# Kernel tuning notes

Measured on AMD Instinct MI355X. Metric: run time of the kernel, lower is better.

Reference implementation:

```python
import jax, jax.numpy as jnp
import numpy as np

EPS = 1e-8


def _mp_match(v1, v2, w):
    """Fused multi-perspective cosine match.
    v1, v2: (G, L, D); w: (P, D). Returns (G, L, P).
    cos_p(l) = <w_p*v1_l, w_p*v2_l> / max(||w_p*v1_l|| * ||w_p*v2_l||, eps)
    """
    w2 = w * w  # (P, D)
    num = jnp.einsum('gld,pd->glp', v1 * v2, w2)
    n1 = jnp.sqrt(jnp.einsum('gld,pd->glp', v1 * v1, w2))
    n2 = jnp.sqrt(jnp.einsum('gld,pd->glp', v2 * v2, w2))
    return num / jnp.maximum(n1 * n2, EPS)


def setup_inputs() -> dict:
    key = jax.random.key(0)
    k1, k2 = jax.random.split(key)
    n_graphs = 64
    nodes_per_graph = 2048
    dim = 128  # must equal perspectives (mp_w is square)
    N = n_graphs * nodes_per_graph
    feats = jax.random.normal(k1, (N, dim), dtype=jnp.float32)
    graph_idx = jnp.repeat(jnp.arange(n_graphs, dtype=jnp.int64), nodes_per_graph)
    mp_w = jax.random.uniform(k2, (dim, dim), dtype=jnp.float32)  # torch.rand
    return {"feats": feats, "mp_w": mp_w, "graph_idx": graph_idx, "n_graphs": n_graphs}


def reference(feats, mp_w, graph_idx, n_graphs):
    N, d = feats.shape
    L = N // n_graphs  # equal-size graphs, graph_idx is sorted/contiguous
    g = feats.reshape(n_graphs, L, d)
    p = g[0::2]  # (G/2, L, d) premise graphs
    h = g[1::2]  # (G/2, L, d) hypothesis graphs
    # cosine_attention is a plain dot product (no normalization in source)
    att = jnp.einsum('gld,gmd->glm', p, h)        # (G/2, Lp, Lh)
    att_p = jnp.einsum('glm,gmd->gld', att, h)     # (G/2, Lp, d)
    att_h = jnp.einsum('glm,gld->gmd', att, p)     # (G/2, Lh, d)
    multi_p = _mp_match(p, att_p, mp_w)            # (G/2, Lp, P)
    multi_h = _mp_match(h, att_h, mp_w)            # (G/2, Lh, P)
    # original concatenates [p0, h0, p1, h1, ...] along node axis
    P = mp_w.shape[0]
    out = jnp.stack([multi_p, multi_h], axis=1).reshape(n_graphs * L, P)
    return out
```

## Files before the change

kernel.cpp:

```cpp
#include <hip/hip_runtime.h>
#include <math.h>

#define D 128
#define GRAPHS 64

typedef __attribute__((ext_vector_type(8))) short bf16x8;
typedef __attribute__((ext_vector_type(4))) float f32x4;

union U4H8 { uint4 u; bf16x8 h; };

__device__ __forceinline__ unsigned short f2bf(float f) {
  union { float f; unsigned u; } v; v.f = f;
  unsigned r = v.u + 0x7fffu + ((v.u >> 16) & 1u);
  return (unsigned short)(r >> 16);
}
__device__ __forceinline__ unsigned asu(float f) {
  union { float f; unsigned u; } v; v.f = f; return v.u;
}
__device__ __forceinline__ float asf(unsigned u) {
  union { unsigned u; float f; } v; v.u = u; return v.f;
}

__global__ __launch_bounds__(256, 2) void gram_partial_kernel(
    const float* __restrict__ feats, unsigned short* __restrict__ partial,
    int L, int KS) {
  const int g = blockIdx.x / KS;
  const int sl = blockIdx.x - g * KS;
  const int chunk = L / KS;
  const float* __restrict__ X = feats + ((size_t)g * L + (size_t)sl * chunk) * D;

  __shared__ __align__(16) unsigned short smem[16384];
  const int tid = threadIdx.x;
  const int wv = tid >> 6, lane = tid & 63, quad = lane >> 4, ln = lane & 15;

  f32x4 acc[2][8];
#pragma unroll
  for (int rt = 0; rt < 2; ++rt)
#pragma unroll
    for (int ct = 0; ct < 8; ++ct) acc[rt][ct] = (f32x4)(0.f);

  int k2v[4], d4v[4];
#pragma unroll
  for (int v = 0; v < 4; ++v) {
    int tt = tid + v * 256;
    k2v[v] = tt & 31;
    d4v[v] = tt >> 5;
  }
  float4 pf[8];
#pragma unroll
  for (int v = 0; v < 4; ++v) {
    pf[2 * v] = *(const float4*)(X + (size_t)(2 * k2v[v]) * D + 4 * d4v[v]);
    pf[2 * v + 1] = *(const float4*)(X + (size_t)(2 * k2v[v] + 1) * D + 4 * d4v[v]);
  }

  for (int it = 0; it < chunk; it += 64) {
    __syncthreads();
#pragma unroll
    for (int v = 0; v < 4; ++v) {
      const float* p0 = (const float*)&pf[2 * v];
      const float* p1 = (const float*)&pf[2 * v + 1];
      int k = 2 * k2v[v];
      int ks = k >> 5, kk = k & 31, qs = kk >> 3, j = kk & 7;
#pragma unroll
      for (int i = 0; i < 4; ++i) {
        int d = 4 * d4v[v] + i, t = d >> 4, lnw = d & 15;
        *(unsigned*)&smem[((ks * 8 + t) * 64 + qs * 16 + lnw) * 8 + j] =
            (unsigned)f2bf(p0[i]) | ((unsigned)f2bf(p1[i]) << 16);
      }
    }
    __syncthreads();
    if (it + 64 < chunk) {
      const float* Xn = X + (size_t)(it + 64) * D;
#pragma unroll
      for (int v = 0; v < 4; ++v) {
        pf[2 * v] = *(const float4*)(Xn + (size_t)(2 * k2v[v]) * D + 4 * d4v[v]);
        pf[2 * v + 1] =
            *(const float4*)(Xn + (size_t)(2 * k2v[v] + 1) * D + 4 * d4v[v]);
      }
    }
#pragma unroll
    for (int ks = 0; ks < 2; ++ks) {
      bf16x8 af[2], bfr[8];
      af[0] = *(const bf16x8*)&smem[((ks * 8 + 2 * wv) * 64 + lane) * 8];
      af[1] = *(const bf16x8*)&smem[((ks * 8 + 2 * wv + 1) * 64 + lane) * 8];
#pragma unroll
      for (int ct = 0; ct < 8; ++ct)
        bfr[ct] = *(const bf16x8*)&smem[((ks * 8 + ct) * 64 + lane) * 8];
#pragma unroll
      for (int rt = 0; rt < 2; ++rt)
#pragma unroll
        for (int ct = 0; ct < 8; ++ct)
          acc[rt][ct] = __builtin_amdgcn_mfma_f32_16x16x32_bf16(
              af[rt], bfr[ct], acc[rt][ct], 0, 0, 0);
    }
  }

  __syncthreads();
#pragma unroll
  for (int rt = 0; rt < 2; ++rt)
#pragma unroll
    for (int ct = 0; ct < 8; ++ct)
#pragma unroll
      for (int r = 0; r < 4; ++r)
        smem[(32 * wv + 16 * rt + quad * 4 + r) * 128 + 16 * ct + ln] =
            f2bf(acc[rt][ct][r]);
  __syncthreads();
  unsigned short* P = partial + ((size_t)sl * GRAPHS + g) * (D * D);
#pragma unroll
  for (int v = 0; v < 8; ++v) {
    int idx = tid + v * 256;
    *(uint4*)&P[(size_t)idx * 8] = *(uint4*)&smem[idx * 8];
  }
}

__global__ __launch_bounds__(256) void reduce_w2_kernel(
    const unsigned short* __restrict__ partial, unsigned short* __restrict__ gram,
    const float* __restrict__ w, unsigned short* __restrict__ w2, int KS) {
  const int bid = blockIdx.x;
  if (bid < 512) {
    int idx = bid * 256 + threadIdx.x;
    int e8 = idx * 8;
    int g = e8 >> 14, e = e8 & (D * D - 1);
    float s[8];
#pragma unroll
    for (int i = 0; i < 8; ++i) s[i] = 0.f;
    for (int sl = 0; sl < KS; ++sl) {
      uint4 t = *(const uint4*)&partial[((size_t)sl * GRAPHS + g) * (D * D) + e];
      const unsigned* tp = &t.x;
#pragma unroll
      for (int q = 0; q < 4; ++q) {
        s[2 * q] += asf(tp[q] << 16);
        s[2 * q + 1] += asf(tp[q] & 0xFFFF0000u);
      }
    }
    uint4 o;
    o.x = (unsigned)f2bf(s[0]) | ((unsigned)f2bf(s[1]) << 16);
    o.y = (unsigned)f2bf(s[2]) | ((unsigned)f2bf(s[3]) << 16);
    o.z = (unsigned)f2bf(s[4]) | ((unsigned)f2bf(s[5]) << 16);
    o.w = (unsigned)f2bf(s[6]) | ((unsigned)f2bf(s[7]) << 16);
    *(uint4*)&gram[(size_t)g * (D * D) + e] = o;
  } else {
    int idx = (bid - 512) * 256 + threadIdx.x;
    const float* src = w + (size_t)idx * 8;
    float4 a = *(const float4*)src;
    float4 b = *(const float4*)(src + 4);
    uint4 o;
    o.x = (unsigned)f2bf(a.x * a.x) | ((unsigned)f2bf(a.y * a.y) << 16);
    o.y = (unsigned)f2bf(a.z * a.z) | ((unsigned)f2bf(a.w * a.w) << 16);
    o.z = (unsigned)f2bf(b.x * b.x) | ((unsigned)f2bf(b.y * b.y) << 16);
    o.w = (unsigned)f2bf(b.z * b.z) | ((unsigned)f2bf(b.w * b.w) << 16);
    *(uint4*)&w2[(size_t)idx * 8] = o;
  }
}

__global__ __launch_bounds__(512, 4) void fused_kernel4(
    const float* __restrict__ feats, const unsigned short* __restrict__ gram,
    const unsigned short* __restrict__ w2, float* __restrict__ out, int L) {
  const int tiles = L >> 6;
  const int gi = blockIdx.x / tiles;
  const int row0 = (blockIdx.x - gi * tiles) << 6;
  const float* __restrict__ A = feats + ((size_t)gi * L + row0) * D;
  const unsigned short* __restrict__ G = gram + (size_t)(gi ^ 1) * (D * D);
  float* __restrict__ O = out + ((size_t)gi * L + row0) * D;

  __shared__ __align__(16) unsigned short sAf[8192];
  __shared__ __align__(16) unsigned short sVf[8192];
  __shared__ __align__(16) unsigned short sBf[16384];

  const int tid = threadIdx.x;
  const int wv = tid >> 6, lane = tid & 63, quad = lane >> 4, ln = lane & 15;
  const int rowg = wv >> 1, colg = wv & 1;

#pragma unroll
  for (int v = 0; v < 4; ++v) {
    int idx = tid + v * 512;
    int r = idx >> 5, c4 = idx & 31;
    float4 t = *(const float4*)(A + (size_t)r * D + c4 * 4);
    int kc = c4 >> 3, qd = (c4 & 7) >> 1, j0 = (c4 & 1) * 4;
    int rt = r >> 4, lnw = r & 15;
    uint2 pk;
    pk.x = (unsigned)f2bf(t.x) | ((unsigned)f2bf(t.y) << 16);
    pk.y = (unsigned)f2bf(t.z) | ((unsigned)f2bf(t.w) << 16);
    *(uint2*)&sAf[((kc * 4 + rt) * 64 + qd * 16 + lnw) * 8 + j0] = pk;
  }
#pragma unroll
  for (int v = 0; v < 4; ++v) {
    int idx = tid + v * 512;
    int r = idx >> 4, c16 = idx & 15;
    uint4 t = *(const uint4*)(G + (size_t)r * D + c16 * 8);
    int kc = c16 >> 2, qd = c16 & 3, tb = r >> 4, lnw = r & 15;
    *(uint4*)&sBf[((kc * 8 + tb) * 64 + qd * 16 + lnw) * 8] = t;
  }
  __syncthreads();

  f32x4 acc1[4];
#pragma unroll
  for (int c = 0; c < 4; ++c) acc1[c] = (f32x4)(0.f);
#pragma unroll
  for (int kc = 0; kc < 4; ++kc) {
    bf16x8 af = *(const bf16x8*)&sAf[((kc * 4 + rowg) * 64 + lane) * 8];
#pragma unroll
    for (int c = 0; c < 4; ++c) {
      int ct = colg * 4 + c;
      bf16x8 bfr = *(const bf16x8*)&sBf[((kc * 8 + ct) * 64 + lane) * 8];
      acc1[c] = __builtin_amdgcn_mfma_f32_16x16x32_bf16(af, bfr, acc1[c], 0, 0, 0);
    }
  }
#pragma unroll
  for (int c = 0; c < 4; ++c)
#pragma unroll
    for (int r = 0; r < 4; ++r) {
      int col = (colg * 4 + c) * 16 + ln;
      int kc_t = col >> 5, q_t = (col >> 3) & 3, j_t = col & 7;
      sVf[((kc_t * 4 + rowg) * 64 + q_t * 16 + quad * 4 + r) * 8 + j_t] =
          f2bf(acc1[c][r]);
    }
  __syncthreads();

#pragma unroll
  for (int v = 0; v < 4; ++v) {
    int idx = tid + v * 512;
    int r = idx >> 4, c16 = idx & 15;
    uint4 t = *(const uint4*)(w2 + (size_t)r * D + c16 * 8);
    int kc = c16 >> 2, qd = c16 & 3, tb = r >> 4, lnw = r & 15;
    *(uint4*)&sBf[((kc * 8 + tb) * 64 + qd * 16 + lnw) * 8] = t;
  }
  __syncthreads();

  f32x4 an[4], s1[4], s2[4];
#pragma unroll
  for (int c = 0; c < 4; ++c) {
    an[c] = (f32x4)(0.f);
    s1[c] = (f32x4)(0.f);
    s2[c] = (f32x4)(0.f);
  }
#pragma unroll
  for (int dc = 0; dc < 4; ++dc) {
    uint4 ua = *(const uint4*)&sAf[((dc * 4 + rowg) * 64 + lane) * 8];
    uint4 uv = *(const uint4*)&sVf[((dc * 4 + rowg) * 64 + lane) * 8];
    U4H8 fx2, faa, fvv;
    const unsigned* uap = &ua.x;
    const unsigned* uvp = &uv.x;
#pragma unroll
    for (int q = 0; q < 4; ++q) {
      float a0 = asf(uap[q] << 16), a1 = asf(uap[q] & 0xFFFF0000u);
      float v0 = asf(uvp[q] << 16), v1 = asf(uvp[q] & 0xFFFF0000u);
      (&fx2.u.x)[q] = __builtin_amdgcn_perm(asu(a1 * v1), asu(a0 * v0), 0x07060302u);
      (&faa.u.x)[q] = __builtin_amdgcn_perm(asu(a1 * a1), asu(a0 * a0), 0x07060302u);
      (&fvv.u.x)[q] = __builtin_amdgcn_perm(asu(v1 * v1), asu(v0 * v0), 0x07060302u);
    }
#pragma unroll
    for (int c = 0; c < 4; ++c) {
      int ct = colg * 4 + c;
      bf16x8 wf = *(const bf16x8*)&sBf[((dc * 8 + ct) * 64 + lane) * 8];
      an[c] = __builtin_amdgcn_mfma_f32_16x16x32_bf16(fx2.h, wf, an[c], 0, 0, 0);
      s1[c] = __builtin_amdgcn_mfma_f32_16x16x32_bf16(faa.h, wf, s1[c], 0, 0, 0);
      s2[c] = __builtin_amdgcn_mfma_f32_16x16x32_bf16(fvv.h, wf, s2[c], 0, 0, 0);
    }
  }

#pragma unroll
  for (int c = 0; c < 4; ++c)
#pragma unroll
    for (int r = 0; r < 4; ++r) {
      float t = fmaxf(s1[c][r] * s2[c][r], 1e-16f);
      O[(size_t)(rowg * 16 + quad * 4 + r) * D + (colg * 4 + c) * 16 + ln] =
          an[c][r] * __builtin_amdgcn_rsqf(t);
    }
}

extern "C" void kernel_launch(void* const* d_in, const int* in_sizes, int n_in,
                              void* d_out, int out_size, void* d_ws, size_t ws_size,
                              hipStream_t stream) {
  const float* feats = (const float*)d_in[0];
  const float* w = (const float*)d_in[1];
  float* out = (float*)d_out;
  const int L = (in_sizes[0] / D) / GRAPHS;

  const size_t partSlice = (size_t)GRAPHS * D * D * sizeof(unsigned short);
  const size_t gramB = partSlice;
  const size_t w2B = (size_t)D * D * sizeof(unsigned short);
  int KS = 4;
  while (KS > 1 && (size_t)KS * partSlice + gramB + w2B > ws_size) KS >>= 1;

  unsigned short* partialBuf = (unsigned short*)d_ws;
  unsigned short* gramBuf = partialBuf + (size_t)KS * GRAPHS * D * D;
  unsigned short* w2Buf = gramBuf + (size_t)GRAPHS * D * D;

  hipLaunchKernelGGL(gram_partial_kernel, dim3(GRAPHS * KS), dim3(256), 0,
                     stream, feats, partialBuf, L, KS);
  hipLaunchKernelGGL(reduce_w2_kernel, dim3(520), dim3(256), 0, stream,
                     partialBuf, gramBuf, w, w2Buf, KS);
  hipLaunchKernelGGL(fused_kernel4, dim3(GRAPHS * (L >> 6)), dim3(512), 0,
                     stream, feats, gramBuf, w2Buf, out, L);
}
```

Baseline: 160.4 us.

## Fuse gram reduction and w-squaring into main kernel, load A fragments directly

Removes the separate reduce/w2 kernel: each fused block now sums the KS partial Gram slices for the partner graph and squares w on the fly, writing both straight into the MFMA-fragment LDS layout. A fragments are loaded from global into registers instead of being staged in LDS. The gram partial kernel stores to LDS in a transposed, packed form, and KS goes from 4 to 8 for more parallelism. The cost is redundant work: every one of the 2048 blocks re-reads KS partial slices and recomputes w squared, which adds global traffic and ALU work per block in exchange for one fewer launch and less LDS.

```diff
diff --git a/kernel.cpp b/kernel.cpp
--- a/kernel.cpp
+++ b/kernel.cpp
@@ -64,7 +64,7 @@
 #pragma unroll
       for (int i = 0; i < 4; ++i) {
         int d = 4 * d4v[v] + i, t = d >> 4, lnw = d & 15;
-        *(unsigned*)&smem[((ks * 8 + t) * 64 + qs * 16 + lnw) * 8 + j] =
+        *(unsigned*)&smem[((ks * 8 + t) * 64 + lnw * 4 + qs) * 8 + j] =
             (unsigned)f2bf(p0[i]) | ((unsigned)f2bf(p1[i]) << 16);
       }
     }
@@ -80,12 +80,13 @@
     }
 #pragma unroll
     for (int ks = 0; ks < 2; ++ks) {
+      const int pos = (ln * 4 + quad) * 8;
       bf16x8 af[2], bfr[8];
-      af[0] = *(const bf16x8*)&smem[((ks * 8 + 2 * wv) * 64 + lane) * 8];
-      af[1] = *(const bf16x8*)&smem[((ks * 8 + 2 * wv + 1) * 64 + lane) * 8];
+      af[0] = *(const bf16x8*)&smem[(ks * 8 + 2 * wv) * 512 + pos];
+      af[1] = *(const bf16x8*)&smem[(ks * 8 + 2 * wv + 1) * 512 + pos];
 #pragma unroll
       for (int ct = 0; ct < 8; ++ct)
-        bfr[ct] = *(const bf16x8*)&smem[((ks * 8 + ct) * 64 + lane) * 8];
+        bfr[ct] = *(const bf16x8*)&smem[(ks * 8 + ct) * 512 + pos];
 #pragma unroll
       for (int rt = 0; rt < 2; ++rt)
 #pragma unroll
@@ -99,11 +100,14 @@
 #pragma unroll
   for (int rt = 0; rt < 2; ++rt)
 #pragma unroll
-    for (int ct = 0; ct < 8; ++ct)
-#pragma unroll
-      for (int r = 0; r < 4; ++r)
-        smem[(32 * wv + 16 * rt + quad * 4 + r) * 128 + 16 * ct + ln] =
-            f2bf(acc[rt][ct][r]);
+    for (int ct = 0; ct < 8; ++ct) {
+      uint2 pk;
+      pk.x = (unsigned)f2bf(acc[rt][ct][0]) |
+             ((unsigned)f2bf(acc[rt][ct][1]) << 16);
+      pk.y = (unsigned)f2bf(acc[rt][ct][2]) |
+             ((unsigned)f2bf(acc[rt][ct][3]) << 16);
+      *(uint2*)&smem[(16 * ct + ln) * 128 + 32 * wv + 16 * rt + quad * 4] = pk;
+    }
   __syncthreads();
   unsigned short* P = partial + ((size_t)sl * GRAPHS + g) * (D * D);
 #pragma unroll
@@ -113,19 +117,48 @@
   }
 }
 
-__global__ __launch_bounds__(256) void reduce_w2_kernel(
-    const unsigned short* __restrict__ partial, unsigned short* __restrict__ gram,
-    const float* __restrict__ w, unsigned short* __restrict__ w2, int KS) {
-  const int bid = blockIdx.x;
-  if (bid < 512) {
-    int idx = bid * 256 + threadIdx.x;
-    int e8 = idx * 8;
-    int g = e8 >> 14, e = e8 & (D * D - 1);
+__global__ __launch_bounds__(512, 4) void fused_kernel5(
+    const float* __restrict__ feats, const unsigned short* __restrict__ partial,
+    const float* __restrict__ w, float* __restrict__ out, int L, int KS) {
+  const int tiles = L >> 6;
+  const int gi = blockIdx.x / tiles;
+  const int row0 = (blockIdx.x - gi * tiles) << 6;
+  const int gx = gi ^ 1;
+  const float* __restrict__ A = feats + ((size_t)gi * L + row0) * D;
+  float* __restrict__ O = out + ((size_t)gi * L + row0) * D;
+
+  __shared__ __align__(16) unsigned short sVf[8192];
+  __shared__ __align__(16) unsigned short sBf[16384];
+
+  const int tid = threadIdx.x;
+  const int wv = tid >> 6, lane = tid & 63, quad = lane >> 4, ln = lane & 15;
+  const int rowg = wv >> 1, colg = wv & 1;
+
+  U4H8 afr[4];
+  {
+    const float* Arow = A + (size_t)(rowg * 16 + ln) * D + quad * 8;
+#pragma unroll
+    for (int kc = 0; kc < 4; ++kc) {
+      float4 t0 = *(const float4*)(Arow + kc * 32);
+      float4 t1 = *(const float4*)(Arow + kc * 32 + 4);
+      afr[kc].u.x = (unsigned)f2bf(t0.x) | ((unsigned)f2bf(t0.y) << 16);
+      afr[kc].u.y = (unsigned)f2bf(t0.z) | ((unsigned)f2bf(t0.w) << 16);
+      afr[kc].u.z = (unsigned)f2bf(t1.x) | ((unsigned)f2bf(t1.y) << 16);
+      afr[kc].u.w = (unsigned)f2bf(t1.z) | ((unsigned)f2bf(t1.w) << 16);
+    }
+  }
+
+#pragma unroll
+  for (int v = 0; v < 4; ++v) {
+    int c = tid + v * 512;
+    int slice = c >> 6, l64 = c & 63;
+    int kc = slice >> 3, tb = slice & 7, qd = l64 >> 4, lnw = l64 & 15;
+    int e = (tb * 16 + lnw) * D + kc * 32 + qd * 8;
     float s[8];
 #pragma unroll
     for (int i = 0; i < 8; ++i) s[i] = 0.f;
-    for (int sl = 0; sl < KS; ++sl) {
-      uint4 t = *(const uint4*)&partial[((size_t)sl * GRAPHS + g) * (D * D) + e];
+    for (int slc = 0; slc < KS; ++slc) {
+      uint4 t = *(const uint4*)&partial[((size_t)slc * GRAPHS + gx) * (D * D) + e];
       const unsigned* tp = &t.x;
 #pragma unroll
       for (int q = 0; q < 4; ++q) {
@@ -138,10 +171,40 @@
     o.y = (unsigned)f2bf(s[2]) | ((unsigned)f2bf(s[3]) << 16);
     o.z = (unsigned)f2bf(s[4]) | ((unsigned)f2bf(s[5]) << 16);
     o.w = (unsigned)f2bf(s[6]) | ((unsigned)f2bf(s[7]) << 16);
-    *(uint4*)&gram[(size_t)g * (D * D) + e] = o;
-  } else {
-    int idx = (bid - 512) * 256 + threadIdx.x;
-    const float* src = w + (size_t)idx * 8;
+    *(uint4*)&sBf[c * 8] = o;
+  }
+  __syncthreads();
+
+  f32x4 acc1[4];
+#pragma unroll
+  for (int c = 0; c < 4; ++c) acc1[c] = (f32x4)(0.f);
+#pragma unroll
+  for (int kc = 0; kc < 4; ++kc) {
+#pragma unroll
+    for (int c = 0; c < 4; ++c) {
+      bf16x8 bfr =
+          *(const bf16x8*)&sBf[((kc * 8 + colg * 4 + c) * 64 + lane) * 8];
+      acc1[c] =
+          __builtin_amdgcn_mfma_f32_16x16x32_bf16(afr[kc].h, bfr, acc1[c], 0, 0, 0);
+    }
+  }
+#pragma unroll
+  for (int c = 0; c < 4; ++c)
+#pragma unroll
+    for (int r = 0; r < 4; ++r) {
+      int col = (colg * 4 + c) * 16 + ln;
+      int kc_t = col >> 5, q_t = (col >> 3) & 3, j_t = col & 7;
+      sVf[((kc_t * 4 + rowg) * 64 + q_t * 16 + quad * 4 + r) * 8 + j_t] =
+          f2bf(acc1[c][r]);
+    }
+  __syncthreads();
+
+#pragma unroll
+  for (int v = 0; v < 4; ++v) {
+    int c = tid + v * 512;
+    int slice = c >> 6, l64 = c & 63;
+    int kc = slice >> 3, tb = slice & 7, qd = l64 >> 4, lnw = l64 & 15;
+    const float* src = w + (size_t)(tb * 16 + lnw) * D + kc * 32 + qd * 8;
     float4 a = *(const float4*)src;
     float4 b = *(const float4*)(src + 4);
     uint4 o;
@@ -149,81 +212,7 @@
     o.y = (unsigned)f2bf(a.z * a.z) | ((unsigned)f2bf(a.w * a.w) << 16);
     o.z = (unsigned)f2bf(b.x * b.x) | ((unsigned)f2bf(b.y * b.y) << 16);
     o.w = (unsigned)f2bf(b.z * b.z) | ((unsigned)f2bf(b.w * b.w) << 16);
-    *(uint4*)&w2[(size_t)idx * 8] = o;
-  }
-}
-
-__global__ __launch_bounds__(512, 4) void fused_kernel4(
-    const float* __restrict__ feats, const unsigned short* __restrict__ gram,
-    const unsigned short* __restrict__ w2, float* __restrict__ out, int L) {
-  const int tiles = L >> 6;
-  const int gi = blockIdx.x / tiles;
-  const int row0 = (blockIdx.x - gi * tiles) << 6;
-  const float* __restrict__ A = feats + ((size_t)gi * L + row0) * D;
-  const unsigned short* __restrict__ G = gram + (size_t)(gi ^ 1) * (D * D);
-  float* __restrict__ O = out + ((size_t)gi * L + row0) * D;
-
-  __shared__ __align__(16) unsigned short sAf[8192];
-  __shared__ __align__(16) unsigned short sVf[8192];
-  __shared__ __align__(16) unsigned short sBf[16384];
-
-  const int tid = threadIdx.x;
-  const int wv = tid >> 6, lane = tid & 63, quad = lane >> 4, ln = lane & 15;
-  const int rowg = wv >> 1, colg = wv & 1;
-
-#pragma unroll
-  for (int v = 0; v < 4; ++v) {
-    int idx = tid + v * 512;
-    int r = idx >> 5, c4 = idx & 31;
-    float4 t = *(const float4*)(A + (size_t)r * D + c4 * 4);
-    int kc = c4 >> 3, qd = (c4 & 7) >> 1, j0 = (c4 & 1) * 4;
-    int rt = r >> 4, lnw = r & 15;
-    uint2 pk;
-    pk.x = (unsigned)f2bf(t.x) | ((unsigned)f2bf(t.y) << 16);
-    pk.y = (unsigned)f2bf(t.z) | ((unsigned)f2bf(t.w) << 16);
-    *(uint2*)&sAf[((kc * 4 + rt) * 64 + qd * 16 + lnw) * 8 + j0] = pk;
-  }
-#pragma unroll
-  for (int v = 0; v < 4; ++v) {
-    int idx = tid + v * 512;
-    int r = idx >> 4, c16 = idx & 15;
-    uint4 t = *(const uint4*)(G + (size_t)r * D + c16 * 8);
-    int kc = c16 >> 2, qd = c16 & 3, tb = r >> 4, lnw = r & 15;
-    *(uint4*)&sBf[((kc * 8 + tb) * 64 + qd * 16 + lnw) * 8] = t;
-  }
-  __syncthreads();
-
-  f32x4 acc1[4];
-#pragma unroll
-  for (int c = 0; c < 4; ++c) acc1[c] = (f32x4)(0.f);
-#pragma unroll
-  for (int kc = 0; kc < 4; ++kc) {
-    bf16x8 af = *(const bf16x8*)&sAf[((kc * 4 + rowg) * 64 + lane) * 8];
-#pragma unroll
-    for (int c = 0; c < 4; ++c) {
-      int ct = colg * 4 + c;
-      bf16x8 bfr = *(const bf16x8*)&sBf[((kc * 8 + ct) * 64 + lane) * 8];
-      acc1[c] = __builtin_amdgcn_mfma_f32_16x16x32_bf16(af, bfr, acc1[c], 0, 0, 0);
-    }
-  }
-#pragma unroll
-  for (int c = 0; c < 4; ++c)
-#pragma unroll
-    for (int r = 0; r < 4; ++r) {
-      int col = (colg * 4 + c) * 16 + ln;
-      int kc_t = col >> 5, q_t = (col >> 3) & 3, j_t = col & 7;
-      sVf[((kc_t * 4 + rowg) * 64 + q_t * 16 + quad * 4 + r) * 8 + j_t] =
-          f2bf(acc1[c][r]);
-    }
-  __syncthreads();
-
-#pragma unroll
-  for (int v = 0; v < 4; ++v) {
-    int idx = tid + v * 512;
-    int r = idx >> 4, c16 = idx & 15;
-    uint4 t = *(const uint4*)(w2 + (size_t)r * D + c16 * 8);
-    int kc = c16 >> 2, qd = c16 & 3, tb = r >> 4, lnw = r & 15;
-    *(uint4*)&sBf[((kc * 8 + tb) * 64 + qd * 16 + lnw) * 8] = t;
+    *(uint4*)&sBf[c * 8] = o;
   }
   __syncthreads();
 
@@ -236,10 +225,9 @@
   }
 #pragma unroll
   for (int dc = 0; dc < 4; ++dc) {
-    uint4 ua = *(const uint4*)&sAf[((dc * 4 + rowg) * 64 + lane) * 8];
     uint4 uv = *(const uint4*)&sVf[((dc * 4 + rowg) * 64 + lane) * 8];
     U4H8 fx2, faa, fvv;
-    const unsigned* uap = &ua.x;
+    const unsigned* uap = &afr[dc].u.x;
     const unsigned* uvp = &uv.x;
 #pragma unroll
     for (int q = 0; q < 4; ++q) {
@@ -251,8 +239,7 @@
     }
 #pragma unroll
     for (int c = 0; c < 4; ++c) {
-      int ct = colg * 4 + c;
-      bf16x8 wf = *(const bf16x8*)&sBf[((dc * 8 + ct) * 64 + lane) * 8];
+      bf16x8 wf = *(const bf16x8*)&sBf[((dc * 8 + colg * 4 + c) * 64 + lane) * 8];
       an[c] = __builtin_amdgcn_mfma_f32_16x16x32_bf16(fx2.h, wf, an[c], 0, 0, 0);
       s1[c] = __builtin_amdgcn_mfma_f32_16x16x32_bf16(faa.h, wf, s1[c], 0, 0, 0);
       s2[c] = __builtin_amdgcn_mfma_f32_16x16x32_bf16(fvv.h, wf, s2[c], 0, 0, 0);
@@ -278,19 +265,13 @@
   const int L = (in_sizes[0] / D) / GRAPHS;
 
   const size_t partSlice = (size_t)GRAPHS * D * D * sizeof(unsigned short);
-  const size_t gramB = partSlice;
-  const size_t w2B = (size_t)D * D * sizeof(unsigned short);
-  int KS = 4;
-  while (KS > 1 && (size_t)KS * partSlice + gramB + w2B > ws_size) KS >>= 1;
+  int KS = 8;
+  while (KS > 1 && (size_t)KS * partSlice > ws_size) KS >>= 1;
 
   unsigned short* partialBuf = (unsigned short*)d_ws;
-  unsigned short* gramBuf = partialBuf + (size_t)KS * GRAPHS * D * D;
-  unsigned short* w2Buf = gramBuf + (size_t)GRAPHS * D * D;
 
   hipLaunchKernelGGL(gram_partial_kernel, dim3(GRAPHS * KS), dim3(256), 0,
                      stream, feats, partialBuf, L, KS);
-  hipLaunchKernelGGL(reduce_w2_kernel, dim3(520), dim3(256), 0, stream,
-                     partialBuf, gramBuf, w, w2Buf, KS);
-  hipLaunchKernelGGL(fused_kernel4, dim3(GRAPHS * (L >> 6)), dim3(512), 0,
-                     stream, feats, gramBuf, w2Buf, out, L);
-}
+  hipLaunchKernelGGL(fused_kernel5, dim3(GRAPHS * (L >> 6)), dim3(512), 0,
+                     stream, feats, partialBuf, w, out, L, KS);
+}
```

After: 217.0 us. 1.35x slower.
